# Optimization experiments

Hardware: AMD Instinct MI355X
Metric: run time of the kernel (lower is better)

The kernel has to match this reference:

```python
import jax, jax.numpy as jnp
import numpy as np


def setup_inputs() -> dict:
    key = jax.random.key(0)
    N, D = 8192, 16384  # tokens x latent dim
    inputs = jax.random.normal(key, (N, D), dtype=jnp.float32)
    return {"inputs": inputs, "k": 64}


def reference(inputs, k):
    # top-k along last axis, then scatter values into a zero tensor
    values, indices = jax.lax.top_k(inputs, k)          # [N, k]
    rows = jnp.arange(inputs.shape[0])[:, None]          # [N, 1]
    sparse = jnp.zeros_like(inputs).at[rows, indices].set(values)
    return sparse
```

## Files before the change

kernel.cpp:

```cpp
#include <hip/hip_runtime.h>

#define BLOCK 256
#define ROW_D 16384
#define VPT (ROW_D / (BLOCK * 4))

__device__ __forceinline__ unsigned keyOf(float f) {
    unsigned u = __float_as_uint(f);
    return (u & 0x80000000u) ? ~u : (u | 0x80000000u);
}
__device__ __forceinline__ float valOf(unsigned m) {
    unsigned u = (m & 0x80000000u) ? (m & 0x7FFFFFFFu) : ~m;
    return __uint_as_float(u);
}

__global__ __launch_bounds__(BLOCK, 4)
void TopKActivation_68324339745162_kernel(const float* __restrict__ in,
                                          float* __restrict__ out,
                                          const int* __restrict__ kptr) {
    __shared__ unsigned hist[256 * 32];
    __shared__ unsigned S[256];
    __shared__ unsigned sDigit, sGreater, sBinCnt, sBase;

    const int t = threadIdx.x;
    const unsigned cpy = (unsigned)t & 31u;
    const size_t rowOff = (size_t)blockIdx.x * (size_t)ROW_D;
    const float4* inRow = reinterpret_cast<const float4*>(in + rowOff);
    float4* outRow = reinterpret_cast<float4*>(out + rowOff);

    uint4 keys[VPT];
#pragma unroll
    for (int j = 0; j < VPT; ++j) {
        float4 v = inRow[t + BLOCK * j];
        keys[j].x = keyOf(v.x);
        keys[j].y = keyOf(v.y);
        keys[j].z = keyOf(v.z);
        keys[j].w = keyOf(v.w);
    }

    unsigned rank = (unsigned)(*kptr);
    unsigned prefix = 0u, pmask = 0u;

    for (int pass = 0; pass < 4; ++pass) {
        const int shift = 24 - 8 * pass;
        for (int i = t; i < 256 * 32; i += BLOCK) hist[i] = 0u;
        __syncthreads();
#pragma unroll
        for (int j = 0; j < VPT; ++j) {
            unsigned kk;
            kk = keys[j].x;
            if ((kk & pmask) == prefix) atomicAdd(&hist[(((kk >> shift) & 255u) << 5) | cpy], 1u);
            kk = keys[j].y;
            if ((kk & pmask) == prefix) atomicAdd(&hist[(((kk >> shift) & 255u) << 5) | cpy], 1u);
            kk = keys[j].z;
            if ((kk & pmask) == prefix) atomicAdd(&hist[(((kk >> shift) & 255u) << 5) | cpy], 1u);
            kk = keys[j].w;
            if ((kk & pmask) == prefix) atomicAdd(&hist[(((kk >> shift) & 255u) << 5) | cpy], 1u);
        }
        __syncthreads();
        unsigned c = 0u;
#pragma unroll
        for (int i = 0; i < 32; ++i) c += hist[((unsigned)t << 5) | (unsigned)((t + i) & 31)];
        S[t] = c;
        __syncthreads();
        for (int step = 1; step < 256; step <<= 1) {
            unsigned v = (t + step < 256) ? S[t + step] : 0u;
            __syncthreads();
            c += v;
            S[t] = c;
            __syncthreads();
        }
        unsigned Snext = (t < 255) ? S[t + 1] : 0u;
        if (c >= rank && Snext < rank) {
            sDigit   = (unsigned)t;
            sGreater = Snext;
            sBinCnt  = c - Snext;
        }
        __syncthreads();
        rank -= sGreater;
        prefix |= sDigit << shift;
        pmask  |= 255u << shift;
    }

    const unsigned T = prefix;
    const unsigned need = rank;
    const bool fastTies = (sBinCnt == need);

    if (fastTies) {
#pragma unroll
        for (int j = 0; j < VPT; ++j) {
            float4 o;
            o.x = (keys[j].x >= T) ? valOf(keys[j].x) : 0.0f;
            o.y = (keys[j].y >= T) ? valOf(keys[j].y) : 0.0f;
            o.z = (keys[j].z >= T) ? valOf(keys[j].z) : 0.0f;
            o.w = (keys[j].w >= T) ? valOf(keys[j].w) : 0.0f;
            outRow[t + BLOCK * j] = o;
        }
    } else {
        if (t == 0) sBase = 0u;
        for (int j = 0; j < VPT; ++j) {
            unsigned lc = (unsigned)(keys[j].x == T) + (unsigned)(keys[j].y == T) +
                          (unsigned)(keys[j].z == T) + (unsigned)(keys[j].w == T);
            __syncthreads();
            S[t] = lc;
            __syncthreads();
            unsigned run = lc;
            for (int step = 1; step < 256; step <<= 1) {
                unsigned v = (t >= step) ? S[t - step] : 0u;
                __syncthreads();
                run += v;
                S[t] = run;
                __syncthreads();
            }
            unsigned r = run - lc + sBase;
            float4 o;
            {
                unsigned kk = keys[j].x;
                if (kk > T) o.x = valOf(kk);
                else if (kk == T) { o.x = (r < need) ? valOf(kk) : 0.0f; ++r; }
                else o.x = 0.0f;
            }
            {
                unsigned kk = keys[j].y;
                if (kk > T) o.y = valOf(kk);
                else if (kk == T) { o.y = (r < need) ? valOf(kk) : 0.0f; ++r; }
                else o.y = 0.0f;
            }
            {
                unsigned kk = keys[j].z;
                if (kk > T) o.z = valOf(kk);
                else if (kk == T) { o.z = (r < need) ? valOf(kk) : 0.0f; ++r; }
                else o.z = 0.0f;
            }
            {
                unsigned kk = keys[j].w;
                if (kk > T) o.w = valOf(kk);
                else if (kk == T) { o.w = (r < need) ? valOf(kk) : 0.0f; ++r; }
                else o.w = 0.0f;
            }
            outRow[t + BLOCK * j] = o;
            __syncthreads();
            if (t == BLOCK - 1) sBase += run;
        }
    }
}

extern "C" void kernel_launch(void* const* d_in, const int* in_sizes, int n_in,
                              void* d_out, int out_size, void* d_ws, size_t ws_size,
                              hipStream_t stream) {
    const float* in = (const float*)d_in[0];
    const int* kptr = (const int*)d_in[1];
    float* out = (float*)d_out;
    const int N = in_sizes[0] / ROW_D;
    TopKActivation_68324339745162_kernel<<<dim3(N), dim3(BLOCK), 0, stream>>>(in, out, kptr);
}
```

Measured before the change: 885.9 us.

## Compact radix-select candidates into shared lists and finish with brute-force rank

After the first 8-bit histogram pass, elements that match the top digit are compacted into a shared list. Later passes build histograms only over that list, using a smaller 8-copy histogram. Once 256 or fewer candidates remain, the threshold is found by a pairwise rank comparison in place of the remaining radix passes. The serial shared-memory scans are replaced with wave-shuffle scans. This cuts the number of barriers and atomics per pass, but adds compaction work and more complex branching.

```diff
diff --git a/kernel.cpp b/kernel.cpp
--- a/kernel.cpp
+++ b/kernel.cpp
@@ -2,7 +2,8 @@
 
 #define BLOCK 256
 #define ROW_D 16384
-#define VPT (ROW_D / (BLOCK * 4))
+#define VPT 16
+#define CAP0 4096
 
 __device__ __forceinline__ unsigned keyOf(float f) {
     unsigned u = __float_as_uint(f);
@@ -11,18 +12,49 @@
 __device__ __forceinline__ float valOf(unsigned m) {
     unsigned u = (m & 0x80000000u) ? (m & 0x7FFFFFFFu) : ~m;
     return __uint_as_float(u);
+}
+
+__device__ __forceinline__ unsigned scanIncl(unsigned v, volatile unsigned* wsum, unsigned t) {
+    unsigned lane = t & 63u, wv = t >> 6;
+    unsigned s = v;
+#pragma unroll
+    for (int d = 1; d < 64; d <<= 1) {
+        unsigned o = __shfl_up(s, (unsigned)d, 64);
+        if (lane >= (unsigned)d) s += o;
+    }
+    __syncthreads();
+    if (lane == 63u) wsum[wv] = s;
+    __syncthreads();
+    unsigned add = 0;
+    for (unsigned w = 0; w < wv; ++w) add += wsum[w];
+    return s + add;
+}
+
+__device__ __forceinline__ unsigned suffixIncl(unsigned v, volatile unsigned* wsum, unsigned t) {
+    unsigned lane = t & 63u, wv = t >> 6;
+    unsigned s = v;
+#pragma unroll
+    for (int d = 1; d < 64; d <<= 1) {
+        unsigned o = __shfl_down(s, (unsigned)d, 64);
+        if (lane + (unsigned)d < 64u) s += o;
+    }
+    __syncthreads();
+    if (lane == 0u) wsum[wv] = s;
+    __syncthreads();
+    unsigned add = 0;
+    for (unsigned w = wv + 1; w < 4u; ++w) add += wsum[w];
+    return s + add;
 }
 
 __global__ __launch_bounds__(BLOCK, 4)
 void TopKActivation_68324339745162_kernel(const float* __restrict__ in,
                                           float* __restrict__ out,
                                           const int* __restrict__ kptr) {
-    __shared__ unsigned hist[256 * 32];
-    __shared__ unsigned S[256];
-    __shared__ unsigned sDigit, sGreater, sBinCnt, sBase;
-
-    const int t = threadIdx.x;
-    const unsigned cpy = (unsigned)t & 31u;
+    __shared__ unsigned pool[8192];
+    __shared__ unsigned wsum[4];
+    __shared__ unsigned sDig, sGr, sCnt, sT, sNeed, sEq, sBase;
+
+    const unsigned t = threadIdx.x;
     const size_t rowOff = (size_t)blockIdx.x * (size_t)ROW_D;
     const float4* inRow = reinterpret_cast<const float4*>(in + rowOff);
     float4* outRow = reinterpret_cast<float4*>(out + rowOff);
@@ -38,53 +70,156 @@
     }
 
     unsigned rank = (unsigned)(*kptr);
-    unsigned prefix = 0u, pmask = 0u;
-
-    for (int pass = 0; pass < 4; ++pass) {
-        const int shift = 24 - 8 * pass;
-        for (int i = t; i < 256 * 32; i += BLOCK) hist[i] = 0u;
-        __syncthreads();
-#pragma unroll
-        for (int j = 0; j < VPT; ++j) {
-            unsigned kk;
-            kk = keys[j].x;
-            if ((kk & pmask) == prefix) atomicAdd(&hist[(((kk >> shift) & 255u) << 5) | cpy], 1u);
-            kk = keys[j].y;
-            if ((kk & pmask) == prefix) atomicAdd(&hist[(((kk >> shift) & 255u) << 5) | cpy], 1u);
-            kk = keys[j].z;
-            if ((kk & pmask) == prefix) atomicAdd(&hist[(((kk >> shift) & 255u) << 5) | cpy], 1u);
-            kk = keys[j].w;
-            if ((kk & pmask) == prefix) atomicAdd(&hist[(((kk >> shift) & 255u) << 5) | cpy], 1u);
-        }
-        __syncthreads();
-        unsigned c = 0u;
-#pragma unroll
-        for (int i = 0; i < 32; ++i) c += hist[((unsigned)t << 5) | (unsigned)((t + i) & 31)];
-        S[t] = c;
-        __syncthreads();
-        for (int step = 1; step < 256; step <<= 1) {
-            unsigned v = (t + step < 256) ? S[t + step] : 0u;
+
+    {
+        uint4* p4 = reinterpret_cast<uint4*>(pool);
+        uint4 z; z.x = z.y = z.z = z.w = 0u;
+#pragma unroll
+        for (int i = 0; i < 8; ++i) p4[t + 256 * i] = z;
+    }
+    __syncthreads();
+    {
+        const unsigned cpy = t & 31u;
+#pragma unroll
+        for (int j = 0; j < VPT; ++j) {
+            atomicAdd(&pool[((keys[j].x >> 24) << 5) | cpy], 1u);
+            atomicAdd(&pool[((keys[j].y >> 24) << 5) | cpy], 1u);
+            atomicAdd(&pool[((keys[j].z >> 24) << 5) | cpy], 1u);
+            atomicAdd(&pool[((keys[j].w >> 24) << 5) | cpy], 1u);
+        }
+    }
+    __syncthreads();
+    unsigned c0 = 0;
+#pragma unroll
+    for (unsigned i = 0; i < 32; ++i) c0 += pool[(t << 5) | ((t + i) & 31u)];
+    {
+        unsigned S = suffixIncl(c0, wsum, t);
+        if (S >= rank && S - c0 < rank) { sDig = t; sGr = S - c0; sCnt = c0; }
+    }
+    __syncthreads();
+    unsigned prefix = sDig << 24;
+    unsigned pmask  = 0xFF000000u;
+    unsigned cnt    = sCnt;
+    rank -= sGr;
+
+    unsigned srcList = 0, listN = 0;
+    if (cnt <= CAP0) {
+        const unsigned dig0 = prefix >> 24;
+        unsigned m = 0;
+#pragma unroll
+        for (int j = 0; j < VPT; ++j) {
+            m += ((keys[j].x >> 24) == dig0);
+            m += ((keys[j].y >> 24) == dig0);
+            m += ((keys[j].z >> 24) == dig0);
+            m += ((keys[j].w >> 24) == dig0);
+        }
+        unsigned incl = scanIncl(m, wsum, t);
+        unsigned pos = incl - m;
+#pragma unroll
+        for (int j = 0; j < VPT; ++j) {
+            if ((keys[j].x >> 24) == dig0) pool[pos++] = keys[j].x;
+            if ((keys[j].y >> 24) == dig0) pool[pos++] = keys[j].y;
+            if ((keys[j].z >> 24) == dig0) pool[pos++] = keys[j].z;
+            if ((keys[j].w >> 24) == dig0) pool[pos++] = keys[j].w;
+        }
+        srcList = 1;
+        listN = cnt;
+        __syncthreads();
+    }
+
+    unsigned* hist1 = pool + 4096;
+    unsigned* list2 = pool + 6144;
+    unsigned T = 0, need = 0, eqc = 0;
+    bool done = false;
+
+    for (int p = 1; p <= 3; ++p) {
+        if (cnt <= 256u) {
+            unsigned m = 0;
+            if (srcList) {
+                for (unsigned i = t; i < listN; i += BLOCK)
+                    m += ((pool[i] & pmask) == prefix);
+            } else {
+#pragma unroll
+                for (int j = 0; j < VPT; ++j) {
+                    m += ((keys[j].x & pmask) == prefix);
+                    m += ((keys[j].y & pmask) == prefix);
+                    m += ((keys[j].z & pmask) == prefix);
+                    m += ((keys[j].w & pmask) == prefix);
+                }
+            }
+            unsigned incl = scanIncl(m, wsum, t);
+            unsigned pos = incl - m;
+            if (srcList) {
+                for (unsigned i = t; i < listN; i += BLOCK) {
+                    unsigned kk = pool[i];
+                    if ((kk & pmask) == prefix) list2[pos++] = kk;
+                }
+            } else {
+#pragma unroll
+                for (int j = 0; j < VPT; ++j) {
+                    if ((keys[j].x & pmask) == prefix) list2[pos++] = keys[j].x;
+                    if ((keys[j].y & pmask) == prefix) list2[pos++] = keys[j].y;
+                    if ((keys[j].z & pmask) == prefix) list2[pos++] = keys[j].z;
+                    if ((keys[j].w & pmask) == prefix) list2[pos++] = keys[j].w;
+                }
+            }
             __syncthreads();
-            c += v;
-            S[t] = c;
+            if (t < cnt) {
+                unsigned x = list2[t];
+                unsigned g = 0, e = 0;
+                for (unsigned j = 0; j < cnt; ++j) {
+                    unsigned y = list2[j];
+                    g += (y > x);
+                    e += (y == x);
+                }
+                if (g < rank && rank <= g + e) { sT = x; sNeed = rank - g; sEq = e; }
+            }
             __syncthreads();
-        }
-        unsigned Snext = (t < 255) ? S[t + 1] : 0u;
-        if (c >= rank && Snext < rank) {
-            sDigit   = (unsigned)t;
-            sGreater = Snext;
-            sBinCnt  = c - Snext;
-        }
-        __syncthreads();
-        rank -= sGreater;
-        prefix |= sDigit << shift;
-        pmask  |= 255u << shift;
-    }
-
-    const unsigned T = prefix;
-    const unsigned need = rank;
-    const bool fastTies = (sBinCnt == need);
-
+            T = sT; need = sNeed; eqc = sEq;
+            done = true;
+            break;
+        }
+
+        const int shift = 24 - 8 * p;
+        {
+            uint4* h4 = reinterpret_cast<uint4*>(hist1);
+            uint4 z; z.x = z.y = z.z = z.w = 0u;
+            h4[2 * t] = z;
+            h4[2 * t + 1] = z;
+        }
+        __syncthreads();
+        const unsigned c8 = t & 7u;
+        if (srcList) {
+            for (unsigned i = t; i < listN; i += BLOCK) {
+                unsigned kk = pool[i];
+                if ((kk & pmask) == prefix)
+                    atomicAdd(&hist1[(((kk >> shift) & 255u) << 3) | c8], 1u);
+            }
+        } else {
+#pragma unroll
+            for (int j = 0; j < VPT; ++j) {
+                unsigned kk;
+                kk = keys[j].x; if ((kk & pmask) == prefix) atomicAdd(&hist1[(((kk >> shift) & 255u) << 3) | c8], 1u);
+                kk = keys[j].y; if ((kk & pmask) == prefix) atomicAdd(&hist1[(((kk >> shift) & 255u) << 3) | c8], 1u);
+                kk = keys[j].z; if ((kk & pmask) == prefix) atomicAdd(&hist1[(((kk >> shift) & 255u) << 3) | c8], 1u);
+                kk = keys[j].w; if ((kk & pmask) == prefix) atomicAdd(&hist1[(((kk >> shift) & 255u) << 3) | c8], 1u);
+            }
+        }
+        __syncthreads();
+        unsigned c = 0;
+#pragma unroll
+        for (unsigned i = 0; i < 8; ++i) c += hist1[(t << 3) | ((t + i) & 7u)];
+        unsigned S = suffixIncl(c, wsum, t);
+        if (S >= rank && S - c < rank) { sDig = t; sGr = S - c; sCnt = c; }
+        __syncthreads();
+        prefix |= (sDig << shift);
+        pmask  |= (255u << shift);
+        cnt = sCnt;
+        rank -= sGr;
+    }
+    if (!done) { T = prefix; need = rank; eqc = cnt; }
+
+    const bool fastTies = (eqc == need);
     if (fastTies) {
 #pragma unroll
         for (int j = 0; j < VPT; ++j) {
@@ -97,21 +232,11 @@
         }
     } else {
         if (t == 0) sBase = 0u;
-        for (int j = 0; j < VPT; ++j) {
-            unsigned lc = (unsigned)(keys[j].x == T) + (unsigned)(keys[j].y == T) +
-                          (unsigned)(keys[j].z == T) + (unsigned)(keys[j].w == T);
-            __syncthreads();
-            S[t] = lc;
-            __syncthreads();
-            unsigned run = lc;
-            for (int step = 1; step < 256; step <<= 1) {
-                unsigned v = (t >= step) ? S[t - step] : 0u;
-                __syncthreads();
-                run += v;
-                S[t] = run;
-                __syncthreads();
-            }
-            unsigned r = run - lc + sBase;
+        __syncthreads();
+        for (int j = 0; j < VPT; ++j) {
+            unsigned lc = (keys[j].x == T) + (keys[j].y == T) + (keys[j].z == T) + (keys[j].w == T);
+            unsigned incl = scanIncl(lc, wsum, t);
+            unsigned r = sBase + incl - lc;
             float4 o;
             {
                 unsigned kk = keys[j].x;
@@ -139,7 +264,7 @@
             }
             outRow[t + BLOCK * j] = o;
             __syncthreads();
-            if (t == BLOCK - 1) sBase += run;
+            if (t == BLOCK - 1) sBase += incl;
         }
     }
 }
```

New measurement: 970.6 us. 9.6% more time.
